# Kernel tuning notes

Hardware: AMD Instinct MI355X
Metric: run time of the kernel (lower is better)

Reference implementation:

```python
import jax, jax.numpy as jnp
import numpy as np

V, D = 100000, 300          # fastText vocab / dim
CV, CD, L = 128, 16, 16     # char vocab / char emb dim / word length
F = 50                      # filters per kernel
KS = (3, 4, 5)              # char CNN kernel widths
H = 150                     # LSTM hidden per direction (2H == D)
FH = 150                    # alpha-encoder FFNN hidden
NF, FE = 64, 50             # entity feature vocab / dim
A = 2000                    # num actors
T = 1024                    # tokens
E = 512                     # entity spans
MAXSPAN = 10                # max span length (ragged -> padded+masked)


def setup_inputs() -> dict:
    key = jax.random.key(0)
    ks = jax.random.split(key, 24)
    g = lambda i, shape, s=0.05: jax.random.normal(ks[i], shape, jnp.float32) * s
    inp = {}
    inp['fast_text'] = g(0, (V, D), 0.1)
    inp['actor_matrix'] = g(1, (A, D), 0.1)
    inp['char_table'] = g(2, (CV, CD), 0.1)
    for j, k in enumerate(KS):
        inp[f'conv_w{k}'] = g(3 + j, (F, CD, k))
        inp[f'conv_b{k}'] = jnp.zeros((F,), jnp.float32)
    din = D + F * len(KS)  # 450 = fastText + char features
    inp['Wi_f'] = g(6, (4 * H, din)); inp['Wh_f'] = g(7, (4 * H, H)); inp['b_f'] = jnp.zeros((4 * H,), jnp.float32)
    inp['Wi_b'] = g(8, (4 * H, din)); inp['Wh_b'] = g(9, (4 * H, H)); inp['b_b'] = jnp.zeros((4 * H,), jnp.float32)
    inp['alpha_W1'] = g(10, (D, FH)); inp['alpha_b1'] = jnp.zeros((FH,), jnp.float32)
    inp['alpha_W2'] = g(11, (FH, FH)); inp['alpha_b2'] = jnp.zeros((FH,), jnp.float32)
    inp['alpha_w_out'] = g(12, (FH,))
    inp['feat_table'] = g(13, (NF, FE), 0.1)
    span_dim = 3 * D + 2 * FE  # 1000, per Model1.span_encoding_dim
    inp['affine_W'] = g(14, (span_dim, D)); inp['affine_b'] = jnp.zeros((D,), jnp.float32)
    inp['word_ids'] = jax.random.randint(ks[15], (T,), 0, V)
    inp['char_ids'] = jax.random.randint(ks[16], (T, L), 0, CV)
    starts = jax.random.randint(ks[17], (E,), 0, T - MAXSPAN)
    lens = jax.random.randint(ks[18], (E,), 1, MAXSPAN + 1)
    feats = jax.random.randint(ks[19], (E, 2), 0, NF)
    inp['espans'] = jnp.concatenate([starts[:, None], (starts + lens)[:, None], feats], axis=1)
    return inp


def _renorm(e):
    # nn.Embedding(max_norm=1.0): renormalize looked-up rows to L2 norm <= 1
    n = jnp.linalg.norm(e, axis=-1, keepdims=True)
    return e * jnp.minimum(1.0, 1.0 / jnp.maximum(n, 1e-7))


def _lstm(x, Wi, Wh, b, reverse):
    Hh = Wh.shape[1]
    def step(carry, xt):
        h, c = carry
        z = xt @ Wi.T + h @ Wh.T + b
        i, f, g2, o = jnp.split(z, 4)
        i = jax.nn.sigmoid(i); f = jax.nn.sigmoid(f)
        g2 = jnp.tanh(g2); o = jax.nn.sigmoid(o)
        c = f * c + i * g2
        h = o * jnp.tanh(c)
        return (h, c), h
    init = (jnp.zeros((Hh,), x.dtype), jnp.zeros((Hh,), x.dtype))
    _, hs = jax.lax.scan(step, init, x, reverse=reverse)
    return hs  # [T, H], hs[i] corresponds to position i


def reference(fast_text, actor_matrix, char_table, conv_w3, conv_b3, conv_w4, conv_b4,
              conv_w5, conv_b5, Wi_f, Wh_f, b_f, Wi_b, Wh_b, b_b,
              alpha_W1, alpha_b1, alpha_W2, alpha_b2, alpha_w_out,
              feat_table, affine_W, affine_b, word_ids, char_ids, espans):
    # --- WordEncoder: fastText + char CNN -> BiLSTM contextual embeddings ---
    ft = fast_text[word_ids]                       # [T, D] fastText embeddings (values)
    ce = char_table[char_ids]                      # [T, L, CD]
    xc = jnp.transpose(ce, (0, 2, 1))              # [T, CD, L]
    feats = []
    for w, bb in ((conv_w3, conv_b3), (conv_w4, conv_b4), (conv_w5, conv_b5)):
        y = jax.lax.conv_general_dilated(xc, w, (1,), 'VALID',
                                         dimension_numbers=('NCW', 'OIW', 'NCW'))
        feats.append(jnp.max(jax.nn.relu(y + bb[None, :, None]), axis=-1))  # [T, F]
    char_feat = jnp.concatenate(feats, axis=-1)    # [T, 150]
    lstm_in = jnp.concatenate([ft, char_feat], axis=-1)  # [T, 450]
    h_f = _lstm(lstm_in, Wi_f, Wh_f, b_f, False)
    h_b = _lstm(lstm_in, Wi_b, Wh_b, b_b, True)
    keys = jnp.concatenate([h_f, h_b], axis=-1)    # [T, D] contextual word embeddings
    values = ft

    # --- espan_encodings: ragged span gather, padded + masked, fully vectorized ---
    s, e = espans[:, 0], espans[:, 1]
    fidx = espans[:, 2:]                           # [E, 2]
    offs = jnp.arange(MAXSPAN)
    idx = jnp.clip(s[:, None] + offs[None, :], 0, keys.shape[0] - 1)  # [E, S]
    mask = offs[None, :] < (e - s)[:, None]        # [E, S]
    k_sp = keys[idx]                               # [E, S, D]
    v_sp = values[idx]                             # [E, S, D]
    # SingleQueryEncoder (alpha_encoder): FFNN scores over keys, softmax-pool values
    hsc = jax.nn.relu(k_sp @ alpha_W1 + alpha_b1)
    hsc = jax.nn.relu(hsc @ alpha_W2 + alpha_b2)
    logits = jnp.where(mask, hsc @ alpha_w_out, -1e30)  # [E, S]
    attn = jax.nn.softmax(logits, axis=-1)
    xh = jnp.einsum('es,esd->ed', attn, v_sp)      # [E, D]
    xf = keys[s]                                   # first token
    xl = keys[e - 1]                               # last token
    fs = _renorm(feat_table[fidx]).reshape(fidx.shape[0], -1)  # [E, 2*FE]
    enc = jnp.concatenate([xf, xl, xh, fs], axis=-1)  # [E, 3D+2FE]

    small = enc @ affine_W + affine_b              # [E, D] affine_ent
    actors = _renorm(actor_matrix)                 # [A, D] actor_embedding max_norm=1
    score_link = actors @ small.T                  # [A, E] DotProduct.simpel
    score_1 = jax.nn.logsumexp(score_link, axis=1) # [A]   Maximum.lse over dim=1
    return score_1, score_link
```

## Files before the change

### kernel.cpp

```cpp
#include <hip/hip_runtime.h>
#include <math.h>

typedef _Float16 h2f __attribute__((ext_vector_type(2)));

__device__ __forceinline__ float fdot2f(h2f a, h2f b, float c) {
#if __has_builtin(__builtin_amdgcn_fdot2)
  return __builtin_amdgcn_fdot2(a, b, c, false);
#else
  return c + (float)a[0] * (float)b[0] + (float)a[1] * (float)b[1];
#endif
}

template <int CTRL>
__device__ __forceinline__ float dpp_f(float x) {
  union { float f; int i; } u, r;
  u.f = x;
  r.i = __builtin_amdgcn_update_dpp(0, u.i, CTRL, 0xF, 0xF, false);
  return r.f;
}

__device__ __forceinline__ float sigf(float x) {
  return __builtin_amdgcn_rcpf(1.f + __expf(-x));
}
__device__ __forceinline__ float tanh_fast(float x) {
  return 2.f * __builtin_amdgcn_rcpf(1.f + __expf(-2.f * x)) - 1.f;
}

__device__ __forceinline__ int clampi(int v, int lo, int hi) {
  return v < lo ? lo : (v > hi ? hi : v);
}

__global__ __launch_bounds__(64) void k_token(
    const float* __restrict__ fast_text, const float* __restrict__ char_table,
    const float* __restrict__ w3, const float* __restrict__ b3,
    const float* __restrict__ w4, const float* __restrict__ b4,
    const float* __restrict__ w5, const float* __restrict__ b5,
    const int* __restrict__ word_ids, const int* __restrict__ char_ids,
    float* __restrict__ lstm_in) {
  const int t = blockIdx.x;
  const int tid = threadIdx.x;
  __shared__ float ce[16][16];
  for (int i = tid; i < 256; i += 64) {
    int l = i >> 4, ci = i & 15;
    ce[l][ci] = char_table[char_ids[t * 16 + l] * 16 + ci];
  }
  __syncthreads();
  const int wid = word_ids[t];
  for (int d = tid; d < 300; d += 64)
    lstm_in[t * 450 + d] = fast_text[wid * 300 + d];
  const int f = tid;
  if (f < 50) {
    {
      float acc[14];
#pragma unroll
      for (int p = 0; p < 14; ++p) acc[p] = 0.f;
      for (int ci = 0; ci < 16; ++ci) {
#pragma unroll
        for (int kk = 0; kk < 3; ++kk) {
          float wv = w3[(f * 16 + ci) * 3 + kk];
#pragma unroll
          for (int p = 0; p < 14; ++p) acc[p] += ce[p + kk][ci] * wv;
        }
      }
      float m = acc[0];
#pragma unroll
      for (int p = 1; p < 14; ++p) m = fmaxf(m, acc[p]);
      lstm_in[t * 450 + 300 + f] = fmaxf(0.f, m + b3[f]);
    }
    {
      float acc[13];
#pragma unroll
      for (int p = 0; p < 13; ++p) acc[p] = 0.f;
      for (int ci = 0; ci < 16; ++ci) {
#pragma unroll
        for (int kk = 0; kk < 4; ++kk) {
          float wv = w4[(f * 16 + ci) * 4 + kk];
#pragma unroll
          for (int p = 0; p < 13; ++p) acc[p] += ce[p + kk][ci] * wv;
        }
      }
      float m = acc[0];
#pragma unroll
      for (int p = 1; p < 13; ++p) m = fmaxf(m, acc[p]);
      lstm_in[t * 450 + 350 + f] = fmaxf(0.f, m + b4[f]);
    }
    {
      float acc[12];
#pragma unroll
      for (int p = 0; p < 12; ++p) acc[p] = 0.f;
      for (int ci = 0; ci < 16; ++ci) {
#pragma unroll
        for (int kk = 0; kk < 5; ++kk) {
          float wv = w5[(f * 16 + ci) * 5 + kk];
#pragma unroll
          for (int p = 0; p < 12; ++p) acc[p] += ce[p + kk][ci] * wv;
        }
      }
      float m = acc[0];
#pragma unroll
      for (int p = 1; p < 12; ++p) m = fmaxf(m, acc[p]);
      lstm_in[t * 450 + 400 + f] = fmaxf(0.f, m + b5[f]);
    }
  }
}

__global__ __launch_bounds__(256) void gemm_nt(
    const float* __restrict__ A, const float* __restrict__ W,
    const float* __restrict__ bias, float* __restrict__ C,
    int M, int N, int K) {
  __shared__ float As[16][64];
  __shared__ float Ws[16][64];
  const int tid = threadIdx.x;
  const int tx = tid & 15, ty = tid >> 4;
  const int r0 = blockIdx.x * 64, c0 = blockIdx.y * 64;
  float acc[4][4] = {};
  for (int k0 = 0; k0 < K; k0 += 16) {
    for (int i = tid; i < 1024; i += 256) {
      int rr = i >> 4, kk = i & 15;
      int r = r0 + rr, k = k0 + kk;
      As[kk][rr] = (r < M && k < K) ? A[r * K + k] : 0.f;
      int c = c0 + rr;
      Ws[kk][rr] = (c < N && k < K) ? W[c * K + k] : 0.f;
    }
    __syncthreads();
#pragma unroll
    for (int kk = 0; kk < 16; ++kk) {
      const float4 av = *(const float4*)(&As[kk][ty * 4]);
      const float4 wv = *(const float4*)(&Ws[kk][tx * 4]);
      float a[4] = {av.x, av.y, av.z, av.w};
      float w[4] = {wv.x, wv.y, wv.z, wv.w};
#pragma unroll
      for (int i = 0; i < 4; ++i)
#pragma unroll
        for (int j = 0; j < 4; ++j) acc[i][j] += a[i] * w[j];
    }
    __syncthreads();
  }
#pragma unroll
  for (int i = 0; i < 4; ++i) {
    int r = r0 + ty * 4 + i;
    if (r >= M) continue;
#pragma unroll
    for (int j = 0; j < 4; ++j) {
      int c = c0 + tx * 4 + j;
      if (c < N) C[r * N + c] = acc[i][j] + (bias ? bias[c] : 0.f);
    }
  }
}

__global__ __launch_bounds__(256) void gemm_xproj(
    const float* __restrict__ A,
    const float* __restrict__ Wf, const float* __restrict__ bf,
    const float* __restrict__ Wb, const float* __restrict__ bb,
    float* __restrict__ xpF, float* __restrict__ xpB) {
  const int M = 1024, N = 600, K = 450;
  const bool back = blockIdx.y >= 10;
  const float* __restrict__ W = back ? Wb : Wf;
  const float* __restrict__ bias = back ? bb : bf;
  float* __restrict__ C = back ? xpB : xpF;
  const int yb = back ? (blockIdx.y - 10) : blockIdx.y;

  __shared__ float As[16][64];
  __shared__ float Ws[16][64];
  const int tid = threadIdx.x;
  const int tx = tid & 15, ty = tid >> 4;
  const int r0 = blockIdx.x * 64, c0 = yb * 64;
  float acc[4][4] = {};
  for (int k0 = 0; k0 < K; k0 += 16) {
    for (int i = tid; i < 1024; i += 256) {
      int rr = i >> 4, kk = i & 15;
      int r = r0 + rr, k = k0 + kk;
      As[kk][rr] = (r < M && k < K) ? A[r * K + k] : 0.f;
      int c = c0 + rr;
      Ws[kk][rr] = (c < N && k < K) ? W[c * K + k] : 0.f;
    }
    __syncthreads();
#pragma unroll
    for (int kk = 0; kk < 16; ++kk) {
      const float4 av = *(const float4*)(&As[kk][ty * 4]);
      const float4 wv = *(const float4*)(&Ws[kk][tx * 4]);
      float a[4] = {av.x, av.y, av.z, av.w};
      float w[4] = {wv.x, wv.y, wv.z, wv.w};
#pragma unroll
      for (int i = 0; i < 4; ++i)
#pragma unroll
        for (int j = 0; j < 4; ++j) acc[i][j] += a[i] * w[j];
    }
    __syncthreads();
  }
#pragma unroll
  for (int i = 0; i < 4; ++i) {
    int r = r0 + ty * 4 + i;
#pragma unroll
    for (int j = 0; j < 4; ++j) {
      int c = c0 + tx * 4 + j;
      if (c < N) C[r * N + c] = acc[i][j] + bias[c];
    }
  }
}

__global__ __launch_bounds__(640, 1) void k_lstm(
    const float* __restrict__ xprojF, const float* __restrict__ xprojB,
    const float* __restrict__ Wh_f, const float* __restrict__ Wh_b,
    float* __restrict__ keys) {
  const int dir = blockIdx.x;
  const float* __restrict__ xp = dir ? xprojB : xprojF;
  const float* __restrict__ Wh = dir ? Wh_b : Wh_f;
  const int tid = threadIdx.x;
  const int u = tid >> 2;
  const int g = tid & 3;
  const int uu = u < 150 ? u : 149;
  const int row = g * 150 + uu;
  const bool act = (tid < 600);

  __shared__ alignas(16) h2f hbuf[2][80];

  h2f w0[20], w1[20], w2[20], w3[20];
  {
    const float* R0 = Wh + (0 * 150 + uu) * 150;
    const float* R1 = Wh + (1 * 150 + uu) * 150;
    const float* R2 = Wh + (2 * 150 + uu) * 150;
    const float* R3 = Wh + (3 * 150 + uu) * 150;
#pragma unroll
    for (int kk = 0; kk < 20; ++kk) {
      const int k = 40 * g + 2 * kk;
      float a0 = 0.f, a1 = 0.f, b0 = 0.f, b1 = 0.f;
      float c0 = 0.f, c1 = 0.f, d0 = 0.f, d1 = 0.f;
      if (k < 150) {
        float2 p;
        p = *(const float2*)(R0 + k); a0 = p.x; a1 = p.y;
        p = *(const float2*)(R1 + k); b0 = p.x; b1 = p.y;
        p = *(const float2*)(R2 + k); c0 = p.x; c1 = p.y;
        p = *(const float2*)(R3 + k); d0 = p.x; d1 = p.y;
      }
      h2f v;
      v[0] = (_Float16)a0; v[1] = (_Float16)a1; w0[kk] = v;
      v[0] = (_Float16)b0; v[1] = (_Float16)b1; w1[kk] = v;
      v[0] = (_Float16)c0; v[1] = (_Float16)c1; w2[kk] = v;
      v[0] = (_Float16)d0; v[1] = (_Float16)d1; w3[kk] = v;
    }
  }
  for (int i = tid; i < 160; i += 640) {
    h2f z;
    z[0] = (_Float16)0.f;
    z[1] = (_Float16)0.f;
    hbuf[i / 80][i % 80] = z;
  }
  float c = 0.f;
  float xv = xp[(dir ? 1023 : 0) * 600 + row];
  __syncthreads();

  int cur = 0;
  for (int step = 0; step < 1024; ++step) {
    const int t = dir ? (1023 - step) : step;
    const int tn = dir ? (t > 0 ? t - 1 : 0) : (t < 1023 ? t + 1 : 1023);
    const float xv_next = xp[tn * 600 + row];
    const float4* hv = (const float4*)hbuf[cur] + 5 * g;
    float a0 = 0.f, a1 = 0.f, a2 = 0.f, a3 = 0.f;
#pragma unroll
    for (int i = 0; i < 5; ++i) {
      float4 q = hv[i];
      const h2f* hh = (const h2f*)&q;
#pragma unroll
      for (int m = 0; m < 4; ++m) {
        a0 = fdot2f(w0[4 * i + m], hh[m], a0);
        a1 = fdot2f(w1[4 * i + m], hh[m], a1);
        a2 = fdot2f(w2[4 * i + m], hh[m], a2);
        a3 = fdot2f(w3[4 * i + m], hh[m], a3);
      }
    }
    const float e0 = a0 + dpp_f<0xB1>(a0);
    const float e1 = a1 + dpp_f<0xB1>(a1);
    const float e2 = a2 + dpp_f<0xB1>(a2);
    const float e3 = a3 + dpp_f<0xB1>(a3);
    const float fa = (g & 1) ? e1 : e0;
    const float fb = (g & 1) ? e3 : e2;
    const float ga_ = fa + dpp_f<0x4E>(fa);
    const float gb_ = fb + dpp_f<0x4E>(fb);
    const float z = ((g & 2) ? gb_ : ga_) + xv;
    xv = xv_next;
    const float zz = (g == 2) ? 2.f * z : z;
    const float s = sigf(zz);
    const float val = (g == 2) ? (2.f * s - 1.f) : s;
    const float v1 = dpp_f<0xB1>(val);
    const float gv = dpp_f<0x4E>(val);
    const float ov = dpp_f<0x4E>(v1);
    if (act && g == 0) {
      c = v1 * c + val * gv;
      const float h = ov * tanh_fast(c);
      keys[t * 300 + dir * 150 + u] = h;
      ((_Float16*)hbuf[cur ^ 1])[u] = (_Float16)h;
    }
    cur ^= 1;
    __syncthreads();
  }
}

__global__ __launch_bounds__(320) void k_span(
    const float* __restrict__ keys, const float* __restrict__ lstm_in,
    const float* __restrict__ W1, const float* __restrict__ b1,
    const float* __restrict__ W2, const float* __restrict__ b2,
    const float* __restrict__ w_out, const float* __restrict__ feat_table,
    const int* __restrict__ espans, float* __restrict__ enc) {
  const int e = blockIdx.x;
  const int tid = threadIdx.x;
  const int s = espans[e * 4 + 0];
  const int en = espans[e * 4 + 1];
  const int f0 = espans[e * 4 + 2];
  const int f1 = espans[e * 4 + 3];

  __shared__ float ksh[10][300];
  __shared__ float hsh[10][152];
  __shared__ float h2sh[10][152];
  __shared__ float att[10];
  __shared__ float scl[2];

  for (int i = tid; i < 3000; i += 320) {
    int p = i / 300, d = i % 300;
    int row = clampi(s + p, 0, 1023);
    ksh[p][d] = keys[row * 300 + d];
  }
  __syncthreads();

  if (tid < 152) {
    int jj = tid;
    if (jj < 150) {
      float acc[10];
#pragma unroll
      for (int p = 0; p < 10; ++p) acc[p] = b1[jj];
      for (int k = 0; k < 300; k += 4) {
        float w0 = W1[(k + 0) * 150 + jj];
        float w1 = W1[(k + 1) * 150 + jj];
        float w2 = W1[(k + 2) * 150 + jj];
        float w3 = W1[(k + 3) * 150 + jj];
#pragma unroll
        for (int p = 0; p < 10; ++p) {
          const float4 kv = *(const float4*)(&ksh[p][k]);
          acc[p] += kv.x * w0 + kv.y * w1 + kv.z * w2 + kv.w * w3;
        }
      }
#pragma unroll
      for (int p = 0; p < 10; ++p) hsh[p][jj] = fmaxf(acc[p], 0.f);
    } else {
#pragma unroll
      for (int p = 0; p < 10; ++p) hsh[p][jj] = 0.f;
    }
  }
  __syncthreads();

  if (tid < 150) {
    int jj = tid;
    float acc[10];
#pragma unroll
    for (int p = 0; p < 10; ++p) acc[p] = b2[jj];
    for (int k = 0; k < 152; k += 4) {
      float w0 = (k + 0 < 150) ? W2[(k + 0) * 150 + jj] : 0.f;
      float w1 = (k + 1 < 150) ? W2[(k + 1) * 150 + jj] : 0.f;
      float w2 = (k + 2 < 150) ? W2[(k + 2) * 150 + jj] : 0.f;
      float w3 = (k + 3 < 150) ? W2[(k + 3) * 150 + jj] : 0.f;
#pragma unroll
      for (int p = 0; p < 10; ++p) {
        const float4 hv = *(const float4*)(&hsh[p][k]);
        acc[p] += hv.x * w0 + hv.y * w1 + hv.z * w2 + hv.w * w3;
      }
    }
#pragma unroll
    for (int p = 0; p < 10; ++p) h2sh[p][jj] = fmaxf(acc[p], 0.f);
  }
  __syncthreads();

  if (tid < 10) {
    float lg = -1e30f;
    if (tid < en - s) {
      float d = 0.f;
      for (int k = 0; k < 150; ++k) d += h2sh[tid][k] * w_out[k];
      lg = d;
    }
    att[tid] = lg;
  }
  if (tid >= 64 && tid < 66) {
    int r = tid - 64;
    int fi = (r == 0) ? f0 : f1;
    float nsq = 0.f;
    for (int k = 0; k < 50; ++k) {
      float v = feat_table[fi * 50 + k];
      nsq += v * v;
    }
    float n = sqrtf(nsq);
    scl[r] = fminf(1.f, 1.f / fmaxf(n, 1e-7f));
  }
  __syncthreads();

  if (tid == 0) {
    float m = -1e30f;
    for (int p = 0; p < 10; ++p) m = fmaxf(m, att[p]);
    float ex[10];
    float ssum = 0.f;
    for (int p = 0; p < 10; ++p) {
      ex[p] = expf(att[p] - m);
      ssum += ex[p];
    }
    for (int p = 0; p < 10; ++p) att[p] = ex[p] / ssum;
  }
  __syncthreads();

  if (tid < 300) {
    int d = tid;
    float xf = keys[s * 300 + d];
    float xl = keys[(en - 1) * 300 + d];
    float xh = 0.f;
#pragma unroll
    for (int p = 0; p < 10; ++p) {
      int row = clampi(s + p, 0, 1023);
      xh += att[p] * lstm_in[row * 450 + d];
    }
    enc[e * 1000 + d] = xf;
    enc[e * 1000 + 300 + d] = xl;
    enc[e * 1000 + 600 + d] = xh;
  }
  if (tid < 100) {
    int r = tid / 50, cc = tid % 50;
    int fi = (r == 0) ? f0 : f1;
    enc[e * 1000 + 900 + tid] = feat_table[fi * 50 + cc] * scl[r];
  }
}

__global__ __launch_bounds__(320) void k_affine(
    const float* __restrict__ enc, const float* __restrict__ W,
    const float* __restrict__ bias, float* __restrict__ small) {
  const int e0 = blockIdx.x * 4;
  const int tid = threadIdx.x;
  __shared__ float es[4][1000];
  for (int i = tid; i < 4000; i += 320) es[i / 1000][i % 1000] = enc[e0 * 1000 + i];
  __syncthreads();
  if (tid < 300) {
    float a0 = bias[tid], a1 = bias[tid], a2 = bias[tid], a3 = bias[tid];
    for (int k = 0; k < 1000; k += 4) {
      float w0 = W[(k + 0) * 300 + tid];
      float w1 = W[(k + 1) * 300 + tid];
      float w2 = W[(k + 2) * 300 + tid];
      float w3 = W[(k + 3) * 300 + tid];
      const float4 v0 = *(const float4*)(&es[0][k]);
      const float4 v1 = *(const float4*)(&es[1][k]);
      const float4 v2 = *(const float4*)(&es[2][k]);
      const float4 v3 = *(const float4*)(&es[3][k]);
      a0 += v0.x * w0 + v0.y * w1 + v0.z * w2 + v0.w * w3;
      a1 += v1.x * w0 + v1.y * w1 + v1.z * w2 + v1.w * w3;
      a2 += v2.x * w0 + v2.y * w1 + v2.z * w2 + v2.w * w3;
      a3 += v3.x * w0 + v3.y * w1 + v3.z * w2 + v3.w * w3;
    }
    small[(e0 + 0) * 300 + tid] = a0;
    small[(e0 + 1) * 300 + tid] = a1;
    small[(e0 + 2) * 300 + tid] = a2;
    small[(e0 + 3) * 300 + tid] = a3;
  }
}

__global__ __launch_bounds__(64) void k_renorm(
    const float* __restrict__ actors, float* __restrict__ actorsN) {
  const int a = blockIdx.x;
  const int l = threadIdx.x;
  float nsq = 0.f;
  for (int d = l; d < 300; d += 64) {
    float v = actors[a * 300 + d];
    nsq += v * v;
  }
  for (int off = 32; off; off >>= 1) nsq += __shfl_down(nsq, off);
  nsq = __shfl(nsq, 0);
  float sc = fminf(1.f, 1.f / fmaxf(sqrtf(nsq), 1e-7f));
  for (int d = l; d < 300; d += 64) actorsN[a * 300 + d] = actors[a * 300 + d] * sc;
}

__global__ __launch_bounds__(64) void k_lse(
    const float* __restrict__ link, float* __restrict__ out) {
  const int a = blockIdx.x;
  const int l = threadIdx.x;
  float v[8];
  float m = -1e30f;
#pragma unroll
  for (int i = 0; i < 8; ++i) {
    v[i] = link[a * 512 + l + i * 64];
    m = fmaxf(m, v[i]);
  }
  for (int off = 32; off; off >>= 1) m = fmaxf(m, __shfl_xor(m, off));
  float ssum = 0.f;
#pragma unroll
  for (int i = 0; i < 8; ++i) ssum += expf(v[i] - m);
  for (int off = 32; off; off >>= 1) ssum += __shfl_xor(ssum, off);
  if (l == 0) out[a] = logf(ssum) + m;
}

extern "C" void kernel_launch(void* const* d_in, const int* in_sizes, int n_in,
                              void* d_out, int out_size, void* d_ws, size_t ws_size,
                              hipStream_t stream) {
  const float* fast_text = (const float*)d_in[0];
  const float* actor_matrix = (const float*)d_in[1];
  const float* char_table = (const float*)d_in[2];
  const float* w3 = (const float*)d_in[3];
  const float* b3 = (const float*)d_in[4];
  const float* w4 = (const float*)d_in[5];
  const float* b4 = (const float*)d_in[6];
  const float* w5 = (const float*)d_in[7];
  const float* b5 = (const float*)d_in[8];
  const float* Wi_f = (const float*)d_in[9];
  const float* Wh_f = (const float*)d_in[10];
  const float* b_f = (const float*)d_in[11];
  const float* Wi_b = (const float*)d_in[12];
  const float* Wh_b = (const float*)d_in[13];
  const float* b_b = (const float*)d_in[14];
  const float* alpha_W1 = (const float*)d_in[15];
  const float* alpha_b1 = (const float*)d_in[16];
  const float* alpha_W2 = (const float*)d_in[17];
  const float* alpha_b2 = (const float*)d_in[18];
  const float* alpha_w_out = (const float*)d_in[19];
  const float* feat_table = (const float*)d_in[20];
  const float* affine_W = (const float*)d_in[21];
  const float* affine_b = (const float*)d_in[22];
  const int* word_ids = (const int*)d_in[23];
  const int* char_ids = (const int*)d_in[24];
  const int* espans = (const int*)d_in[25];

  float* ws = (float*)d_ws;
  float* lstm_in = ws;
  float* xpF = lstm_in + 460800;
  float* xpB = xpF + 614400;
  float* keys = xpB + 614400;
  float* enc = keys + 307200;
  float* small = enc + 512000;
  float* actN = small + 153600;

  float* out = (float*)d_out;
  float* score_link = out + 2000;

  k_token<<<1024, 64, 0, stream>>>(fast_text, char_table, w3, b3, w4, b4, w5, b5,
                                   word_ids, char_ids, lstm_in);
  gemm_xproj<<<dim3(16, 20), 256, 0, stream>>>(lstm_in, Wi_f, b_f, Wi_b, b_b,
                                               xpF, xpB);
  k_lstm<<<2, 640, 0, stream>>>(xpF, xpB, Wh_f, Wh_b, keys);
  k_renorm<<<2000, 64, 0, stream>>>(actor_matrix, actN);
  k_span<<<512, 320, 0, stream>>>(keys, lstm_in, alpha_W1, alpha_b1, alpha_W2,
                                  alpha_b2, alpha_w_out, feat_table, espans, enc);
  k_affine<<<128, 320, 0, stream>>>(enc, affine_W, affine_b, small);
  gemm_nt<<<dim3(32, 8), 256, 0, stream>>>(actN, small, nullptr, score_link,
                                           2000, 512, 300);
  k_lse<<<2000, 64, 0, stream>>>(score_link, out);
}
```

Baseline: 1.131 ms.

## Run LSTM recurrent matvec on bf16 MFMA with register-resident weight fragments

Rewrites the sequential LSTM kernel so that each of 4 waves holds bf16 fragments of the recurrent weights for three 16-unit tiles and computes the Wh·h product with v_mfma_f32_16x16x32_bf16 each step. This replaces the fp16 dot2 plus DPP reductions across 640 threads. The hidden state is broadcast through shared memory in bf16, and gate activations are computed per lane from the selected accumulator element. The goal is to shorten per-step latency on the serial 1024-step critical path, at the cost of bf16 precision and much of each MFMA's work being discarded as padding, since only one column of h is used.

```diff
diff --git a/kernel.cpp b/kernel.cpp
--- a/kernel.cpp
+++ b/kernel.cpp
@@ -1,22 +1,14 @@
 #include <hip/hip_runtime.h>
 #include <math.h>
 
-typedef _Float16 h2f __attribute__((ext_vector_type(2)));
-
-__device__ __forceinline__ float fdot2f(h2f a, h2f b, float c) {
-#if __has_builtin(__builtin_amdgcn_fdot2)
-  return __builtin_amdgcn_fdot2(a, b, c, false);
-#else
-  return c + (float)a[0] * (float)b[0] + (float)a[1] * (float)b[1];
-#endif
-}
-
-template <int CTRL>
-__device__ __forceinline__ float dpp_f(float x) {
-  union { float f; int i; } u, r;
-  u.f = x;
-  r.i = __builtin_amdgcn_update_dpp(0, u.i, CTRL, 0xF, 0xF, false);
-  return r.f;
+typedef __attribute__((ext_vector_type(4))) float f32x4;
+typedef __attribute__((ext_vector_type(8))) short bf16x8;
+
+__device__ __forceinline__ unsigned short f2bf(float x) {
+  union { float f; unsigned u; } v;
+  v.f = x;
+  unsigned r = v.u + 0x7FFF + ((v.u >> 16) & 1);
+  return (unsigned short)(r >> 16);
 }
 
 __device__ __forceinline__ float sigf(float x) {
@@ -24,6 +16,12 @@
 }
 __device__ __forceinline__ float tanh_fast(float x) {
   return 2.f * __builtin_amdgcn_rcpf(1.f + __expf(-2.f * x)) - 1.f;
+}
+
+__device__ __forceinline__ float zsel(f32x4 c, int jj) {
+  float ab = (jj & 1) ? c.y : c.x;
+  float cd = (jj & 1) ? c.w : c.z;
+  return (jj & 2) ? cd : ab;
 }
 
 __device__ __forceinline__ int clampi(int v, int lo, int hi) {
@@ -199,7 +197,7 @@
   }
 }
 
-__global__ __launch_bounds__(640, 1) void k_lstm(
+__global__ __launch_bounds__(256, 1) void k_lstm(
     const float* __restrict__ xprojF, const float* __restrict__ xprojB,
     const float* __restrict__ Wh_f, const float* __restrict__ Wh_b,
     float* __restrict__ keys) {
@@ -207,89 +205,101 @@
   const float* __restrict__ xp = dir ? xprojB : xprojF;
   const float* __restrict__ Wh = dir ? Wh_b : Wh_f;
   const int tid = threadIdx.x;
-  const int u = tid >> 2;
-  const int g = tid & 3;
-  const int uu = u < 150 ? u : 149;
-  const int row = g * 150 + uu;
-  const bool act = (tid < 600);
-
-  __shared__ alignas(16) h2f hbuf[2][80];
-
-  h2f w0[20], w1[20], w2[20], w3[20];
-  {
-    const float* R0 = Wh + (0 * 150 + uu) * 150;
-    const float* R1 = Wh + (1 * 150 + uu) * 150;
-    const float* R2 = Wh + (2 * 150 + uu) * 150;
-    const float* R3 = Wh + (3 * 150 + uu) * 150;
-#pragma unroll
-    for (int kk = 0; kk < 20; ++kk) {
-      const int k = 40 * g + 2 * kk;
-      float a0 = 0.f, a1 = 0.f, b0 = 0.f, b1 = 0.f;
-      float c0 = 0.f, c1 = 0.f, d0 = 0.f, d1 = 0.f;
-      if (k < 150) {
-        float2 p;
-        p = *(const float2*)(R0 + k); a0 = p.x; a1 = p.y;
-        p = *(const float2*)(R1 + k); b0 = p.x; b1 = p.y;
-        p = *(const float2*)(R2 + k); c0 = p.x; c1 = p.y;
-        p = *(const float2*)(R3 + k); d0 = p.x; d1 = p.y;
-      }
-      h2f v;
-      v[0] = (_Float16)a0; v[1] = (_Float16)a1; w0[kk] = v;
-      v[0] = (_Float16)b0; v[1] = (_Float16)b1; w1[kk] = v;
-      v[0] = (_Float16)c0; v[1] = (_Float16)c1; w2[kk] = v;
-      v[0] = (_Float16)d0; v[1] = (_Float16)d1; w3[kk] = v;
-    }
-  }
-  for (int i = tid; i < 160; i += 640) {
-    h2f z;
-    z[0] = (_Float16)0.f;
-    z[1] = (_Float16)0.f;
-    hbuf[i / 80][i % 80] = z;
-  }
-  float c = 0.f;
-  float xv = xp[(dir ? 1023 : 0) * 600 + row];
+  const int w = tid >> 6;
+  const int l = tid & 63;
+  const int r16 = l & 15;
+  const int ch = l >> 4;
+  const int jj = l & 3;
+
+  __shared__ alignas(16) unsigned short hb[2][192];
+
+  bf16x8 A[3][4][5];
+#pragma unroll
+  for (int Ti = 0; Ti < 3; ++Ti) {
+    const int T = w * 3 + Ti;
+    const int u = T * 16 + r16;
+#pragma unroll
+    for (int g = 0; g < 4; ++g) {
+      const float* Wr = Wh + (g * 150 + (u < 150 ? u : 0)) * 150;
+#pragma unroll
+      for (int kt = 0; kt < 5; ++kt) {
+        const int k0 = kt * 32 + ch * 8;
+        float vals[8];
+#pragma unroll
+        for (int j2 = 0; j2 < 4; ++j2) {
+          const int k = k0 + j2 * 2;
+          if (u < 150 && k < 150) {
+            float2 p = *(const float2*)(Wr + k);
+            vals[j2 * 2] = p.x;
+            vals[j2 * 2 + 1] = p.y;
+          } else {
+            vals[j2 * 2] = 0.f;
+            vals[j2 * 2 + 1] = 0.f;
+          }
+        }
+        bf16x8 s;
+#pragma unroll
+        for (int j = 0; j < 8; ++j) s[j] = (short)f2bf(vals[j]);
+        A[Ti][g][kt] = s;
+      }
+    }
+  }
+
+  for (int i = tid; i < 2 * 192; i += 256) hb[i / 192][i % 192] = 0;
+  float cst[3] = {0.f, 0.f, 0.f};
   __syncthreads();
 
   int cur = 0;
   for (int step = 0; step < 1024; ++step) {
     const int t = dir ? (1023 - step) : step;
-    const int tn = dir ? (t > 0 ? t - 1 : 0) : (t < 1023 ? t + 1 : 1023);
-    const float xv_next = xp[tn * 600 + row];
-    const float4* hv = (const float4*)hbuf[cur] + 5 * g;
-    float a0 = 0.f, a1 = 0.f, a2 = 0.f, a3 = 0.f;
-#pragma unroll
-    for (int i = 0; i < 5; ++i) {
-      float4 q = hv[i];
-      const h2f* hh = (const h2f*)&q;
-#pragma unroll
-      for (int m = 0; m < 4; ++m) {
-        a0 = fdot2f(w0[4 * i + m], hh[m], a0);
-        a1 = fdot2f(w1[4 * i + m], hh[m], a1);
-        a2 = fdot2f(w2[4 * i + m], hh[m], a2);
-        a3 = fdot2f(w3[4 * i + m], hh[m], a3);
-      }
-    }
-    const float e0 = a0 + dpp_f<0xB1>(a0);
-    const float e1 = a1 + dpp_f<0xB1>(a1);
-    const float e2 = a2 + dpp_f<0xB1>(a2);
-    const float e3 = a3 + dpp_f<0xB1>(a3);
-    const float fa = (g & 1) ? e1 : e0;
-    const float fb = (g & 1) ? e3 : e2;
-    const float ga_ = fa + dpp_f<0x4E>(fa);
-    const float gb_ = fb + dpp_f<0x4E>(fb);
-    const float z = ((g & 2) ? gb_ : ga_) + xv;
-    xv = xv_next;
-    const float zz = (g == 2) ? 2.f * z : z;
-    const float s = sigf(zz);
-    const float val = (g == 2) ? (2.f * s - 1.f) : s;
-    const float v1 = dpp_f<0xB1>(val);
-    const float gv = dpp_f<0x4E>(val);
-    const float ov = dpp_f<0x4E>(v1);
-    if (act && g == 0) {
-      c = v1 * c + val * gv;
-      const float h = ov * tanh_fast(c);
-      keys[t * 300 + dir * 150 + u] = h;
-      ((_Float16*)hbuf[cur ^ 1])[u] = (_Float16)h;
+
+    float xpv[3][4];
+#pragma unroll
+    for (int Ti = 0; Ti < 3; ++Ti) {
+      const int u = (w * 3 + Ti) * 16 + ch * 4 + jj;
+      const int uc = u < 150 ? u : 149;
+#pragma unroll
+      for (int g = 0; g < 4; ++g) xpv[Ti][g] = xp[t * 600 + g * 150 + uc];
+    }
+
+    f32x4 Cf[3][4];
+#pragma unroll
+    for (int Ti = 0; Ti < 3; ++Ti)
+#pragma unroll
+      for (int g = 0; g < 4; ++g) Cf[Ti][g] = (f32x4){0.f, 0.f, 0.f, 0.f};
+
+#pragma unroll
+    for (int kt = 0; kt < 5; ++kt) {
+      union { float4 f; bf16x8 s; } cv;
+      cv.f = *(const float4*)((const char*)&hb[cur][0] + kt * 64 + ch * 16);
+      const bf16x8 b = cv.s;
+#pragma unroll
+      for (int Ti = 0; Ti < 3; ++Ti)
+#pragma unroll
+        for (int g = 0; g < 4; ++g)
+          asm volatile("v_mfma_f32_16x16x32_bf16 %0, %1, %2, %0"
+                       : "+a"(Cf[Ti][g])
+                       : "a"(A[Ti][g][kt]), "v"(b));
+    }
+    asm volatile("s_nop 7\n\ts_nop 7\n\ts_nop 7");
+
+#pragma unroll
+    for (int Ti = 0; Ti < 3; ++Ti) {
+      const int u = (w * 3 + Ti) * 16 + ch * 4 + jj;
+      const float zi = zsel(Cf[Ti][0], jj) + xpv[Ti][0];
+      const float zf = zsel(Cf[Ti][1], jj) + xpv[Ti][1];
+      const float zg = zsel(Cf[Ti][2], jj) + xpv[Ti][2];
+      const float zo = zsel(Cf[Ti][3], jj) + xpv[Ti][3];
+      const float ig = sigf(zi);
+      const float fg = sigf(zf);
+      const float gg = tanh_fast(zg);
+      const float og = sigf(zo);
+      cst[Ti] = fg * cst[Ti] + ig * gg;
+      const float h = og * tanh_fast(cst[Ti]);
+      if ((l & 12) == 0 && u < 150) {
+        hb[cur ^ 1][u] = f2bf(h);
+        keys[t * 300 + dir * 150 + u] = h;
+      }
     }
     cur ^= 1;
     __syncthreads();
@@ -323,16 +333,16 @@
   __syncthreads();
 
   if (tid < 152) {
-    int jj = tid;
-    if (jj < 150) {
+    int jjj = tid;
+    if (jjj < 150) {
       float acc[10];
 #pragma unroll
-      for (int p = 0; p < 10; ++p) acc[p] = b1[jj];
+      for (int p = 0; p < 10; ++p) acc[p] = b1[jjj];
       for (int k = 0; k < 300; k += 4) {
-        float w0 = W1[(k + 0) * 150 + jj];
-        float w1 = W1[(k + 1) * 150 + jj];
-        float w2 = W1[(k + 2) * 150 + jj];
-        float w3 = W1[(k + 3) * 150 + jj];
+        float w0 = W1[(k + 0) * 150 + jjj];
+        float w1 = W1[(k + 1) * 150 + jjj];
+        float w2 = W1[(k + 2) * 150 + jjj];
+        float w3 = W1[(k + 3) * 150 + jjj];
 #pragma unroll
         for (int p = 0; p < 10; ++p) {
           const float4 kv = *(const float4*)(&ksh[p][k]);
@@ -340,24 +350,24 @@
         }
       }
 #pragma unroll
-      for (int p = 0; p < 10; ++p) hsh[p][jj] = fmaxf(acc[p], 0.f);
+      for (int p = 0; p < 10; ++p) hsh[p][jjj] = fmaxf(acc[p], 0.f);
     } else {
 #pragma unroll
-      for (int p = 0; p < 10; ++p) hsh[p][jj] = 0.f;
+      for (int p = 0; p < 10; ++p) hsh[p][jjj] = 0.f;
     }
   }
   __syncthreads();
 
   if (tid < 150) {
-    int jj = tid;
+    int jjj = tid;
     float acc[10];
 #pragma unroll
-    for (int p = 0; p < 10; ++p) acc[p] = b2[jj];
+    for (int p = 0; p < 10; ++p) acc[p] = b2[jjj];
     for (int k = 0; k < 152; k += 4) {
-      float w0 = (k + 0 < 150) ? W2[(k + 0) * 150 + jj] : 0.f;
-      float w1 = (k + 1 < 150) ? W2[(k + 1) * 150 + jj] : 0.f;
-      float w2 = (k + 2 < 150) ? W2[(k + 2) * 150 + jj] : 0.f;
-      float w3 = (k + 3 < 150) ? W2[(k + 3) * 150 + jj] : 0.f;
+      float w0 = (k + 0 < 150) ? W2[(k + 0) * 150 + jjj] : 0.f;
+      float w1 = (k + 1 < 150) ? W2[(k + 1) * 150 + jjj] : 0.f;
+      float w2 = (k + 2 < 150) ? W2[(k + 2) * 150 + jjj] : 0.f;
+      float w3 = (k + 3 < 150) ? W2[(k + 3) * 150 + jjj] : 0.f;
 #pragma unroll
       for (int p = 0; p < 10; ++p) {
         const float4 hv = *(const float4*)(&hsh[p][k]);
@@ -365,7 +375,7 @@
       }
     }
 #pragma unroll
-    for (int p = 0; p < 10; ++p) h2sh[p][jj] = fmaxf(acc[p], 0.f);
+    for (int p = 0; p < 10; ++p) h2sh[p][jjj] = fmaxf(acc[p], 0.f);
   }
   __syncthreads();
 
@@ -536,7 +546,7 @@
                                    word_ids, char_ids, lstm_in);
   gemm_xproj<<<dim3(16, 20), 256, 0, stream>>>(lstm_in, Wi_f, b_f, Wi_b, b_b,
                                                xpF, xpB);
-  k_lstm<<<2, 640, 0, stream>>>(xpF, xpB, Wh_f, Wh_b, keys);
+  k_lstm<<<2, 256, 0, stream>>>(xpF, xpB, Wh_f, Wh_b, keys);
   k_renorm<<<2000, 64, 0, stream>>>(actor_matrix, actN);
   k_span<<<512, 320, 0, stream>>>(keys, lstm_in, alpha_W1, alpha_b1, alpha_W2,
                                   alpha_b2, alpha_w_out, feat_table, espans, enc);
```

Measured after the change: 1.846 ms. 63.2% more time.

## Restructure LSTM recurrence: each thread owns three full gate rows, shared-memory gate exchange

Applied to the files above, without the earlier changes.

The recurrent LSTM kernel drops from 640 threads, where four lanes split each gate row's dot product and combined partial sums with DPP shuffles, to 256 threads. Each of these threads holds three complete Wh rows in registers (225 half2 values) and computes their full dot products. Gate pre-activations are written to shared memory and a second barrier-separated phase applies the cell update on 150 threads. This removes the cross-lane reductions and uses fewer waves, but adds an extra __syncthreads per step, a longer serial dot product per thread, and heavy register pressure that may spill.

```diff
diff --git a/kernel.cpp b/kernel.cpp
--- a/kernel.cpp
+++ b/kernel.cpp
@@ -9,14 +9,6 @@
 #else
   return c + (float)a[0] * (float)b[0] + (float)a[1] * (float)b[1];
 #endif
-}
-
-template <int CTRL>
-__device__ __forceinline__ float dpp_f(float x) {
-  union { float f; int i; } u, r;
-  u.f = x;
-  r.i = __builtin_amdgcn_update_dpp(0, u.i, CTRL, 0xF, 0xF, false);
-  return r.f;
 }
 
 __device__ __forceinline__ float sigf(float x) {
@@ -199,7 +191,7 @@
   }
 }
 
-__global__ __launch_bounds__(640, 1) void k_lstm(
+__global__ __launch_bounds__(256, 1) void k_lstm(
     const float* __restrict__ xprojF, const float* __restrict__ xprojB,
     const float* __restrict__ Wh_f, const float* __restrict__ Wh_b,
     float* __restrict__ keys) {
@@ -207,89 +199,89 @@
   const float* __restrict__ xp = dir ? xprojB : xprojF;
   const float* __restrict__ Wh = dir ? Wh_b : Wh_f;
   const int tid = threadIdx.x;
-  const int u = tid >> 2;
-  const int g = tid & 3;
-  const int uu = u < 150 ? u : 149;
-  const int row = g * 150 + uu;
-  const bool act = (tid < 600);
+  const int i3 = tid < 200 ? tid : 199;
+  const int r0 = 3 * i3;
 
   __shared__ alignas(16) h2f hbuf[2][80];
-
-  h2f w0[20], w1[20], w2[20], w3[20];
+  __shared__ float zsh[600];
+
+  h2f wA[75], wB[75], wC[75];
   {
-    const float* R0 = Wh + (0 * 150 + uu) * 150;
-    const float* R1 = Wh + (1 * 150 + uu) * 150;
-    const float* R2 = Wh + (2 * 150 + uu) * 150;
-    const float* R3 = Wh + (3 * 150 + uu) * 150;
-#pragma unroll
-    for (int kk = 0; kk < 20; ++kk) {
-      const int k = 40 * g + 2 * kk;
-      float a0 = 0.f, a1 = 0.f, b0 = 0.f, b1 = 0.f;
-      float c0 = 0.f, c1 = 0.f, d0 = 0.f, d1 = 0.f;
-      if (k < 150) {
-        float2 p;
-        p = *(const float2*)(R0 + k); a0 = p.x; a1 = p.y;
-        p = *(const float2*)(R1 + k); b0 = p.x; b1 = p.y;
-        p = *(const float2*)(R2 + k); c0 = p.x; c1 = p.y;
-        p = *(const float2*)(R3 + k); d0 = p.x; d1 = p.y;
-      }
+    const float2* RA = (const float2*)(Wh + (r0 + 0) * 150);
+    const float2* RB = (const float2*)(Wh + (r0 + 1) * 150);
+    const float2* RC = (const float2*)(Wh + (r0 + 2) * 150);
+#pragma unroll
+    for (int kk = 0; kk < 75; ++kk) {
+      float2 a = RA[kk], b = RB[kk], d = RC[kk];
       h2f v;
-      v[0] = (_Float16)a0; v[1] = (_Float16)a1; w0[kk] = v;
-      v[0] = (_Float16)b0; v[1] = (_Float16)b1; w1[kk] = v;
-      v[0] = (_Float16)c0; v[1] = (_Float16)c1; w2[kk] = v;
-      v[0] = (_Float16)d0; v[1] = (_Float16)d1; w3[kk] = v;
-    }
-  }
-  for (int i = tid; i < 160; i += 640) {
+      v[0] = (_Float16)a.x; v[1] = (_Float16)a.y; wA[kk] = v;
+      v[0] = (_Float16)b.x; v[1] = (_Float16)b.y; wB[kk] = v;
+      v[0] = (_Float16)d.x; v[1] = (_Float16)d.y; wC[kk] = v;
+    }
+  }
+  for (int i = tid; i < 160; i += 256) {
     h2f z;
     z[0] = (_Float16)0.f;
     z[1] = (_Float16)0.f;
     hbuf[i / 80][i % 80] = z;
   }
   float c = 0.f;
-  float xv = xp[(dir ? 1023 : 0) * 600 + row];
+  const int t0 = dir ? 1023 : 0;
+  float xvA = xp[t0 * 600 + r0 + 0];
+  float xvB = xp[t0 * 600 + r0 + 1];
+  float xvC = xp[t0 * 600 + r0 + 2];
   __syncthreads();
 
   int cur = 0;
   for (int step = 0; step < 1024; ++step) {
     const int t = dir ? (1023 - step) : step;
     const int tn = dir ? (t > 0 ? t - 1 : 0) : (t < 1023 ? t + 1 : 1023);
-    const float xv_next = xp[tn * 600 + row];
-    const float4* hv = (const float4*)hbuf[cur] + 5 * g;
-    float a0 = 0.f, a1 = 0.f, a2 = 0.f, a3 = 0.f;
-#pragma unroll
-    for (int i = 0; i < 5; ++i) {
-      float4 q = hv[i];
-      const h2f* hh = (const h2f*)&q;
+    const float xnA = xp[tn * 600 + r0 + 0];
+    const float xnB = xp[tn * 600 + r0 + 1];
+    const float xnC = xp[tn * 600 + r0 + 2];
+    const float4* hv = (const float4*)hbuf[cur];
+    float aA = 0.f, aB = 0.f, aC = 0.f;
+#pragma unroll
+    for (int q = 0; q < 18; ++q) {
+      float4 hq = hv[q];
+      const h2f* hh = (const h2f*)&hq;
 #pragma unroll
       for (int m = 0; m < 4; ++m) {
-        a0 = fdot2f(w0[4 * i + m], hh[m], a0);
-        a1 = fdot2f(w1[4 * i + m], hh[m], a1);
-        a2 = fdot2f(w2[4 * i + m], hh[m], a2);
-        a3 = fdot2f(w3[4 * i + m], hh[m], a3);
-      }
-    }
-    const float e0 = a0 + dpp_f<0xB1>(a0);
-    const float e1 = a1 + dpp_f<0xB1>(a1);
-    const float e2 = a2 + dpp_f<0xB1>(a2);
-    const float e3 = a3 + dpp_f<0xB1>(a3);
-    const float fa = (g & 1) ? e1 : e0;
-    const float fb = (g & 1) ? e3 : e2;
-    const float ga_ = fa + dpp_f<0x4E>(fa);
-    const float gb_ = fb + dpp_f<0x4E>(fb);
-    const float z = ((g & 2) ? gb_ : ga_) + xv;
-    xv = xv_next;
-    const float zz = (g == 2) ? 2.f * z : z;
-    const float s = sigf(zz);
-    const float val = (g == 2) ? (2.f * s - 1.f) : s;
-    const float v1 = dpp_f<0xB1>(val);
-    const float gv = dpp_f<0x4E>(val);
-    const float ov = dpp_f<0x4E>(v1);
-    if (act && g == 0) {
-      c = v1 * c + val * gv;
-      const float h = ov * tanh_fast(c);
-      keys[t * 300 + dir * 150 + u] = h;
-      ((_Float16*)hbuf[cur ^ 1])[u] = (_Float16)h;
+        aA = fdot2f(wA[4 * q + m], hh[m], aA);
+        aB = fdot2f(wB[4 * q + m], hh[m], aB);
+        aC = fdot2f(wC[4 * q + m], hh[m], aC);
+      }
+    }
+    {
+      float4 hq = hv[18];
+      const h2f* hh = (const h2f*)&hq;
+#pragma unroll
+      for (int m = 0; m < 3; ++m) {
+        aA = fdot2f(wA[72 + m], hh[m], aA);
+        aB = fdot2f(wB[72 + m], hh[m], aB);
+        aC = fdot2f(wC[72 + m], hh[m], aC);
+      }
+    }
+    if (tid < 200) {
+      zsh[r0 + 0] = aA + xvA;
+      zsh[r0 + 1] = aB + xvB;
+      zsh[r0 + 2] = aC + xvC;
+    }
+    xvA = xnA; xvB = xnB; xvC = xnC;
+    __syncthreads();
+    if (tid < 150) {
+      const float zi = zsh[tid];
+      const float zf = zsh[150 + tid];
+      const float zg = zsh[300 + tid];
+      const float zo = zsh[450 + tid];
+      const float ig = sigf(zi);
+      const float fg = sigf(zf);
+      const float gg = tanh_fast(zg);
+      const float og = sigf(zo);
+      c = fg * c + ig * gg;
+      const float h = og * tanh_fast(c);
+      keys[t * 300 + dir * 150 + tid] = h;
+      ((_Float16*)hbuf[cur ^ 1])[tid] = (_Float16)h;
     }
     cur ^= 1;
     __syncthreads();
@@ -536,7 +528,7 @@
                                    word_ids, char_ids, lstm_in);
   gemm_xproj<<<dim3(16, 20), 256, 0, stream>>>(lstm_in, Wi_f, b_f, Wi_b, b_b,
                                                xpF, xpB);
-  k_lstm<<<2, 640, 0, stream>>>(xpF, xpB, Wh_f, Wh_b, keys);
+  k_lstm<<<2, 256, 0, stream>>>(xpF, xpB, Wh_f, Wh_b, keys);
   k_renorm<<<2000, 64, 0, stream>>>(actor_matrix, actN);
   k_span<<<512, 320, 0, stream>>>(keys, lstm_in, alpha_W1, alpha_b1, alpha_W2,
                                   alpha_b2, alpha_w_out, feat_table, espans, enc);
```

New measurement: 1.183 ms. 4.6% more time.
